# Kernel optimization log

Hardware: AMD Instinct MI355X
Metric: run time of the kernel (lower is better)

Reference implementation:

```python
import jax, jax.numpy as jnp
import numpy as np

N_NODES = 20000
N_EDGES = 640000
NUM_FEATURES = 128
HIDDEN = 256
NUM_CLASSES = 40
EPS = 0.0  # GINConv default eps, not trained


def gin_conv(x, edge_index, W, b):
    # sum-aggregate neighbor features: messages flow src -> dst
    src, dst = edge_index[0], edge_index[1]
    agg = jax.ops.segment_sum(x[src], dst, num_segments=N_NODES)  # [N, d]
    h = (1.0 + EPS) * x + agg
    return h @ W + b


def setup_inputs() -> dict:
    key = jax.random.key(0)
    ks = jax.random.split(key, 10)
    x = jax.random.normal(ks[0], (N_NODES, NUM_FEATURES), dtype=jnp.float32)
    edge_index = jax.random.randint(ks[1], (2, N_EDGES), 0, N_NODES, dtype=jnp.int64)

    def lin(k, fan_in, fan_out):
        kw, kb = jax.random.split(k)
        lim = 1.0 / np.sqrt(fan_in)
        W = jax.random.uniform(kw, (fan_in, fan_out), jnp.float32, -lim, lim)
        b = jax.random.uniform(kb, (fan_out,), jnp.float32, -lim, lim)
        return W, b

    W1, b1 = lin(ks[2], NUM_FEATURES, HIDDEN)
    W2, b2 = lin(ks[3], HIDDEN, HIDDEN)
    W3, b3 = lin(ks[4], HIDDEN, HIDDEN)
    W4, b4 = lin(ks[5], HIDDEN, NUM_CLASSES)
    return {"x": x, "edge_index": edge_index,
            "W1": W1, "b1": b1, "W2": W2, "b2": b2,
            "W3": W3, "b3": b3, "W4": W4, "b4": b4}


def reference(x, edge_index, W1, b1, W2, b2, W3, b3, W4, b4):
    h = jax.nn.relu(gin_conv(x, edge_index, W1, b1))
    h = jax.nn.relu(gin_conv(h, edge_index, W2, b2))
    h = jax.nn.relu(gin_conv(h, edge_index, W3, b3))
    return gin_conv(h, edge_index, W4, b4)
```

## Files before the change

kernel.cpp:

```cpp
#include <hip/hip_runtime.h>

typedef __attribute__((ext_vector_type(8))) short bf16x8;
typedef __attribute__((ext_vector_type(4))) float f32x4;
typedef __attribute__((ext_vector_type(2))) float f32x2;

#define CAP 128

__device__ __forceinline__ ushort f2bf(float f) {
    union { float f; uint u; } c; c.f = f;
    uint u = c.u;
    u += 0x7fffu + ((u >> 16) & 1u);
    return (ushort)(u >> 16);
}
__device__ __forceinline__ f32x2 up2(uint u) {
    union { uint u; float f; } lo, hi;
    lo.u = u << 16; hi.u = u & 0xffff0000u;
    f32x2 r; r.x = lo.f; r.y = hi.f; return r;
}
__device__ __forceinline__ void acc4(f32x2* a, uint4 v) {
    a[0] += up2(v.x); a[1] += up2(v.y); a[2] += up2(v.z); a[3] += up2(v.w);
}

__global__ void zero_kernel(int* __restrict__ p, int n) {
    int i = blockIdx.x * blockDim.x + threadIdx.x;
    if (i < n) p[i] = 0;
}

__global__ void fill_cvt(const int* __restrict__ src, const int* __restrict__ dst,
                         int* __restrict__ cnt, ushort* __restrict__ pcsr, int E,
                         const float* __restrict__ x, ushort* __restrict__ xb, int n4,
                         const float* __restrict__ W1, ushort* __restrict__ W1T,
                         const float* __restrict__ W2, ushort* __restrict__ W2T,
                         const float* __restrict__ W3, ushort* __restrict__ W3T,
                         const float* __restrict__ W4, ushort* __restrict__ W4T) {
    int idx = blockIdx.x * blockDim.x + threadIdx.x;
    if (idx < E) {
        int d = dst[idx];
        int pos = atomicAdd(&cnt[d], 1);
        pcsr[((size_t)d << 7) + pos] = (ushort)src[idx];
        return;
    }
    idx -= E;
    if (idx < n4) {
        float4 v = *(const float4*)&x[(size_t)idx * 4];
        ushort4 o; o.x = f2bf(v.x); o.y = f2bf(v.y); o.z = f2bf(v.z); o.w = f2bf(v.w);
        *(ushort4*)&xb[(size_t)idx * 4] = o;
        return;
    }
    int i = idx - n4;
    if (i < 32768) {
        int n = i & 255, k = i >> 8;
        W1T[n * 128 + k] = f2bf(W1[k * 256 + n]);
    } else if (i < 32768 + 65536) {
        int j = i - 32768; int n = j & 255, k = j >> 8;
        W2T[n * 256 + k] = f2bf(W2[k * 256 + n]);
    } else if (i < 32768 + 131072) {
        int j = i - 98304; int n = j & 255, k = j >> 8;
        W3T[n * 256 + k] = f2bf(W3[k * 256 + n]);
    } else if (i < 32768 + 131072 + 32768) {
        int j = i - 163840; int n = j & 127, k = j >> 7;
        W4T[n * 256 + k] = f2bf(n < 40 ? W4[k * 40 + n] : 0.f);
    }
}

template <int D>
__global__ __launch_bounds__(256) void gather_chunk(
        const ushort* __restrict__ xb, const int* __restrict__ cnt,
        const ushort* __restrict__ pcsr, ushort* __restrict__ h, int N) {
    constexpr int CF = D / 4;
    constexpr int LPN = CF / 8;
    constexpr int NPB = 256 / LPN;
    constexpr int RS = (D == 256) ? 9 : 8;
    int chunk = blockIdx.x & 3;
    int t = threadIdx.x;
    int node = (blockIdx.x >> 2) * NPB + (t / LPN);
    if (node >= N) return;
    int l = t & (LPN - 1);
    uint fo2 = (uint)chunk * (CF * 2) + (uint)l * 16;
    const char* xc = (const char*)xb;
    char* hc = (char*)h;
    int deg = cnt[node];
    const ushort* crow = pcsr + ((size_t)node << 7);
    uint selfoff = ((uint)node << RS) + fo2;

    f32x2 a[4], b[4] = {}, c[4] = {}, d[4] = {};
    {
        uint4 sv = *(const uint4*)(xc + selfoff);
        a[0] = up2(sv.x); a[1] = up2(sv.y); a[2] = up2(sv.z); a[3] = up2(sv.w);
    }
    int e = 0;
    for (; e + 4 <= deg; e += 4) {
        uint s0 = crow[e], s1 = crow[e + 1], s2 = crow[e + 2], s3 = crow[e + 3];
        uint4 v0 = *(const uint4*)(xc + (s0 << RS) + fo2);
        uint4 v1 = *(const uint4*)(xc + (s1 << RS) + fo2);
        uint4 v2 = *(const uint4*)(xc + (s2 << RS) + fo2);
        uint4 v3 = *(const uint4*)(xc + (s3 << RS) + fo2);
        acc4(a, v0); acc4(b, v1); acc4(c, v2); acc4(d, v3);
    }
    for (; e < deg; ++e) {
        uint s = crow[e];
        uint4 v = *(const uint4*)(xc + (s << RS) + fo2);
        acc4(a, v);
    }
    #pragma unroll
    for (int i = 0; i < 4; ++i) a[i] += (b[i] + c[i]) + d[i];
    uint4 o;
    o.x = (uint)f2bf(a[0].x) | ((uint)f2bf(a[0].y) << 16);
    o.y = (uint)f2bf(a[1].x) | ((uint)f2bf(a[1].y) << 16);
    o.z = (uint)f2bf(a[2].x) | ((uint)f2bf(a[2].y) << 16);
    o.w = (uint)f2bf(a[3].x) | ((uint)f2bf(a[3].y) << 16);
    *(uint4*)(hc + selfoff) = o;
}

__global__ __launch_bounds__(256) void gather_out_kernel(
        const ushort* __restrict__ y, const int* __restrict__ cnt,
        const ushort* __restrict__ pcsr, const float* __restrict__ b,
        float* __restrict__ out, int N) {
    int node = blockIdx.x * 32 + (threadIdx.x >> 3);
    if (node >= N) return;
    int l = threadIdx.x & 7;
    uint fo2 = (uint)l * 16;
    const char* yc = (const char*)y;
    int deg = cnt[node];
    const ushort* crow = pcsr + ((size_t)node << 7);

    f32x2 a[4], bb[4] = {}, cc[4] = {}, dd[4] = {};
    {
        uint4 sv = *(const uint4*)(yc + ((uint)node << 7) + fo2);
        a[0] = up2(sv.x); a[1] = up2(sv.y); a[2] = up2(sv.z); a[3] = up2(sv.w);
    }
    int e = 0;
    for (; e + 4 <= deg; e += 4) {
        uint s0 = crow[e], s1 = crow[e + 1], s2 = crow[e + 2], s3 = crow[e + 3];
        uint4 v0 = *(const uint4*)(yc + (s0 << 7) + fo2);
        uint4 v1 = *(const uint4*)(yc + (s1 << 7) + fo2);
        uint4 v2 = *(const uint4*)(yc + (s2 << 7) + fo2);
        uint4 v3 = *(const uint4*)(yc + (s3 << 7) + fo2);
        acc4(a, v0); acc4(bb, v1); acc4(cc, v2); acc4(dd, v3);
    }
    for (; e < deg; ++e) {
        uint s = crow[e];
        uint4 v = *(const uint4*)(yc + (s << 7) + fo2);
        acc4(a, v);
    }
    #pragma unroll
    for (int i = 0; i < 4; ++i) a[i] += (bb[i] + cc[i]) + dd[i];

    if (l < 5) {
        int f = l * 8;
        float4 o0 = make_float4(a[0].x + b[f + 0], a[0].y + b[f + 1],
                                a[1].x + b[f + 2], a[1].y + b[f + 3]);
        float4 o1 = make_float4(a[2].x + b[f + 4], a[2].y + b[f + 5],
                                a[3].x + b[f + 6], a[3].y + b[f + 7]);
        *(float4*)&out[(size_t)node * 40 + f] = o0;
        *(float4*)&out[(size_t)node * 40 + f + 4] = o1;
    }
}

#define GBM 64
#define GBN 128
#define GBK 64
#define LDT 72

template <bool OUTF32, bool RELU>
__global__ __launch_bounds__(256) void mfma_gemm(
        const ushort* __restrict__ A, const ushort* __restrict__ BT,
        const float* __restrict__ bias, void* __restrict__ Cout,
        int M, int Ncols, int K, int Cld) {
    __shared__ __align__(16) ushort As[GBM * LDT];
    __shared__ __align__(16) ushort Bs[GBN * LDT];
    int tid = threadIdx.x;
    int lane = tid & 63;
    int wave = tid >> 6;
    int row0 = blockIdx.x * GBM;
    int col0 = blockIdx.y * GBN;
    int wr = (wave >> 1) * 32;
    int wc = (wave & 1) * 64;
    int sr = tid >> 3;
    int sc = (tid & 7) * 8;
    int rr = lane & 15;
    int kq = (lane >> 4) * 8;
    f32x4 acc[2][4] = {};

    for (int k0 = 0; k0 < K; k0 += GBK) {
        int4 a0 = *(const int4*)&A[(size_t)(row0 + sr) * K + k0 + sc];
        int4 a1 = *(const int4*)&A[(size_t)(row0 + sr + 32) * K + k0 + sc];
        int4 b0 = *(const int4*)&BT[(size_t)(col0 + sr) * K + k0 + sc];
        int4 b1 = *(const int4*)&BT[(size_t)(col0 + sr + 32) * K + k0 + sc];
        int4 b2 = *(const int4*)&BT[(size_t)(col0 + sr + 64) * K + k0 + sc];
        int4 b3 = *(const int4*)&BT[(size_t)(col0 + sr + 96) * K + k0 + sc];
        __syncthreads();
        *(int4*)&As[sr * LDT + sc] = a0;
        *(int4*)&As[(sr + 32) * LDT + sc] = a1;
        *(int4*)&Bs[sr * LDT + sc] = b0;
        *(int4*)&Bs[(sr + 32) * LDT + sc] = b1;
        *(int4*)&Bs[(sr + 64) * LDT + sc] = b2;
        *(int4*)&Bs[(sr + 96) * LDT + sc] = b3;
        __syncthreads();
        #pragma unroll
        for (int kk = 0; kk < 2; ++kk) {
            int kof = kk * 32 + kq;
            bf16x8 af[2], bfr[4];
            #pragma unroll
            for (int i = 0; i < 2; ++i)
                af[i] = *(const bf16x8*)&As[(wr + i * 16 + rr) * LDT + kof];
            #pragma unroll
            for (int j = 0; j < 4; ++j)
                bfr[j] = *(const bf16x8*)&Bs[(wc + j * 16 + rr) * LDT + kof];
            #pragma unroll
            for (int i = 0; i < 2; ++i)
                #pragma unroll
                for (int j = 0; j < 4; ++j)
                    acc[i][j] = __builtin_amdgcn_mfma_f32_16x16x32_bf16(af[i], bfr[j], acc[i][j], 0, 0, 0);
        }
    }

    int rq = (lane >> 4) * 4;
    #pragma unroll
    for (int j = 0; j < 4; ++j) {
        int col = col0 + wc + j * 16 + rr;
        if (col >= Ncols) continue;
        float bv = bias ? bias[col] : 0.f;
        #pragma unroll
        for (int i = 0; i < 2; ++i) {
            #pragma unroll
            for (int r = 0; r < 4; ++r) {
                int row = row0 + wr + i * 16 + rq + r;
                if (row >= M) continue;
                float v = acc[i][j][r] + bv;
                if (RELU) v = fmaxf(v, 0.f);
                if (OUTF32) ((float*)Cout)[(size_t)row * Cld + col] = v;
                else        ((ushort*)Cout)[(size_t)row * Cld + col] = f2bf(v);
            }
        }
    }
}

static inline size_t al256(size_t x) { return (x + 255) & ~(size_t)255; }

extern "C" void kernel_launch(void* const* d_in, const int* in_sizes, int n_in,
                              void* d_out, int out_size, void* d_ws, size_t ws_size,
                              hipStream_t stream) {
    const float* x  = (const float*)d_in[0];
    const int*   ei = (const int*)d_in[1];
    const float* W1 = (const float*)d_in[2];
    const float* b1 = (const float*)d_in[3];
    const float* W2 = (const float*)d_in[4];
    const float* b2 = (const float*)d_in[5];
    const float* W3 = (const float*)d_in[6];
    const float* b3 = (const float*)d_in[7];
    const float* W4 = (const float*)d_in[8];
    const float* b4 = (const float*)d_in[9];
    float* out = (float*)d_out;

    int N = in_sizes[0] / 128;
    int E = in_sizes[1] / 2;
    const int* src = ei;
    const int* dst = ei + E;
    int Mpad = ((N + 127) / 128) * 128;

    char* ws = (char*)d_ws;
    int* cnt       = (int*)ws;
    ushort* pcsr   = (ushort*)(cnt + N);
    size_t off = al256((size_t)N * 4 + (size_t)N * CAP * 2);
    ushort* xb   = (ushort*)(ws + off); off += al256((size_t)N * 128 * 2);
    ushort* bufH = (ushort*)(ws + off); off += al256((size_t)Mpad * 256 * 2);
    ushort* bufA = (ushort*)(ws + off); off += al256((size_t)Mpad * 256 * 2);
    ushort* bufB = (ushort*)(ws + off); off += al256((size_t)Mpad * 256 * 2);
    ushort* bufY = (ushort*)(ws + off); off += al256((size_t)Mpad * 64 * 2);
    ushort* W1T  = (ushort*)(ws + off); off += al256((size_t)256 * 128 * 2);
    ushort* W2T  = (ushort*)(ws + off); off += al256((size_t)256 * 256 * 2);
    ushort* W3T  = (ushort*)(ws + off); off += al256((size_t)256 * 256 * 2);
    ushort* W4T  = (ushort*)(ws + off); off += al256((size_t)128 * 256 * 2);

    zero_kernel<<<(N + 1023) / 1024, 1024, 0, stream>>>(cnt, N);

    int n4 = N * 128 / 4;
    int fcTotal = E + n4 + 196608;
    fill_cvt<<<(fcTotal + 255) / 256, 256, 0, stream>>>(src, dst, cnt, pcsr, E, x, xb, n4,
                                                        W1, W1T, W2, W2T, W3, W3T, W4, W4T);

    int g1Blocks = ((N + 63) / 64) * 4;
    int g2Blocks = ((N + 31) / 32) * 4;
    dim3 gemmGrid(Mpad / GBM, 2);
    dim3 gemmGrid4(Mpad / GBM, 1);

    gather_chunk<128><<<g1Blocks, 256, 0, stream>>>(xb, cnt, pcsr, bufH, N);
    mfma_gemm<false, true><<<gemmGrid, 256, 0, stream>>>(bufH, W1T, b1, bufA, N, 256, 128, 256);
    gather_chunk<256><<<g2Blocks, 256, 0, stream>>>(bufA, cnt, pcsr, bufH, N);
    mfma_gemm<false, true><<<gemmGrid, 256, 0, stream>>>(bufH, W2T, b2, bufB, N, 256, 256, 256);
    gather_chunk<256><<<g2Blocks, 256, 0, stream>>>(bufB, cnt, pcsr, bufH, N);
    mfma_gemm<false, true><<<gemmGrid, 256, 0, stream>>>(bufH, W3T, b3, bufA, N, 256, 256, 256);
    mfma_gemm<false, false><<<gemmGrid4, 256, 0, stream>>>(bufA, W4T, nullptr, bufY, N, 64, 256, 64);
    gather_out_kernel<<<(N + 31) / 32, 256, 0, stream>>>(bufY, cnt, pcsr, b4, out, N);
}
```

Before: 178.4 us.

## Split CSR build atomics into 8 partitioned counters then compact

Edge insertion now spreads atomics over 8 counter partitions chosen by block index, writing into per-partition 32-slot segments. A new compact kernel prefix-sums the partition counts and copies them into the original padded CSR. The aim is to reduce atomic contention on the per-node counters. In exchange it adds a kernel launch, more zeroing and extra memory traffic, and a node can overflow a 32-slot partition segment.

```diff
diff --git a/kernel.cpp b/kernel.cpp
--- a/kernel.cpp
+++ b/kernel.cpp
@@ -5,6 +5,7 @@
 typedef __attribute__((ext_vector_type(2))) float f32x2;
 
 #define CAP 128
+#define SEGC 32
 
 __device__ __forceinline__ ushort f2bf(float f) {
     union { float f; uint u; } c; c.f = f;
@@ -27,7 +28,7 @@
 }
 
 __global__ void fill_cvt(const int* __restrict__ src, const int* __restrict__ dst,
-                         int* __restrict__ cnt, ushort* __restrict__ pcsr, int E,
+                         int* __restrict__ cnt8, ushort* __restrict__ pseg, int E, int N,
                          const float* __restrict__ x, ushort* __restrict__ xb, int n4,
                          const float* __restrict__ W1, ushort* __restrict__ W1T,
                          const float* __restrict__ W2, ushort* __restrict__ W2T,
@@ -35,9 +36,10 @@
                          const float* __restrict__ W4, ushort* __restrict__ W4T) {
     int idx = blockIdx.x * blockDim.x + threadIdx.x;
     if (idx < E) {
+        int p = blockIdx.x & 7;
         int d = dst[idx];
-        int pos = atomicAdd(&cnt[d], 1);
-        pcsr[((size_t)d << 7) + pos] = (ushort)src[idx];
+        int pos = atomicAdd(&cnt8[p * N + d], 1);
+        pseg[((size_t)d << 8) + (p << 5) + pos] = (ushort)src[idx];
         return;
     }
     idx -= E;
@@ -61,6 +63,24 @@
         int j = i - 163840; int n = j & 127, k = j >> 7;
         W4T[n * 256 + k] = f2bf(n < 40 ? W4[k * 40 + n] : 0.f);
     }
+}
+
+__global__ __launch_bounds__(256) void compact_kernel(
+        const int* __restrict__ cnt8, const ushort* __restrict__ pseg,
+        int* __restrict__ cnt, ushort* __restrict__ pcsr, int N) {
+    int node = blockIdx.x * 32 + (threadIdx.x >> 3);
+    if (node >= N) return;
+    int p = threadIdx.x & 7;
+    int c[8];
+    #pragma unroll
+    for (int q = 0; q < 8; ++q) c[q] = cnt8[q * N + node];
+    int pre = 0;
+    #pragma unroll
+    for (int q = 0; q < 8; ++q) if (q < p) pre += c[q];
+    const ushort* srow = pseg + ((size_t)node << 8) + (p << 5);
+    ushort* drow = pcsr + ((size_t)node << 7) + pre;
+    for (int i = 0; i < c[p]; ++i) drow[i] = srow[i];
+    if (p == 7) cnt[node] = pre + c[7];
 }
 
 template <int D>
@@ -260,9 +280,11 @@
     int Mpad = ((N + 127) / 128) * 128;
 
     char* ws = (char*)d_ws;
-    int* cnt       = (int*)ws;
-    ushort* pcsr   = (ushort*)(cnt + N);
-    size_t off = al256((size_t)N * 4 + (size_t)N * CAP * 2);
+    int* cnt8      = (int*)ws;
+    int* cnt       = cnt8 + 8 * N;
+    ushort* pseg   = (ushort*)(cnt + N);
+    ushort* pcsr   = pseg + (size_t)N * 256;
+    size_t off = al256((size_t)(9 * N) * 4 + (size_t)N * 256 * 2 + (size_t)N * CAP * 2);
     ushort* xb   = (ushort*)(ws + off); off += al256((size_t)N * 128 * 2);
     ushort* bufH = (ushort*)(ws + off); off += al256((size_t)Mpad * 256 * 2);
     ushort* bufA = (ushort*)(ws + off); off += al256((size_t)Mpad * 256 * 2);
@@ -273,12 +295,13 @@
     ushort* W3T  = (ushort*)(ws + off); off += al256((size_t)256 * 256 * 2);
     ushort* W4T  = (ushort*)(ws + off); off += al256((size_t)128 * 256 * 2);
 
-    zero_kernel<<<(N + 1023) / 1024, 1024, 0, stream>>>(cnt, N);
+    zero_kernel<<<(8 * N + 1023) / 1024, 1024, 0, stream>>>(cnt8, 8 * N);
 
     int n4 = N * 128 / 4;
     int fcTotal = E + n4 + 196608;
-    fill_cvt<<<(fcTotal + 255) / 256, 256, 0, stream>>>(src, dst, cnt, pcsr, E, x, xb, n4,
+    fill_cvt<<<(fcTotal + 255) / 256, 256, 0, stream>>>(src, dst, cnt8, pseg, E, N, x, xb, n4,
                                                         W1, W1T, W2, W2T, W3, W3T, W4, W4T);
+    compact_kernel<<<(N + 31) / 32, 256, 0, stream>>>(cnt8, pseg, cnt, pcsr, N);
 
     int g1Blocks = ((N + 63) / 64) * 4;
     int g2Blocks = ((N + 31) / 32) * 4;
```

Result: no change. 175.4 us (-1.7%).

## Build padded CSR via two-pass bucketed binning with shared-memory atomics

Applied to the files above, without the earlier changes.

Replaces the zero kernel plus global-atomic CSR fill with a two-pass scheme. First, edge blocks bin edges into 64-node buckets using LDS atomics and write packed (dst,src) pairs to a staging region. Second, one block per bucket scatters them into the padded CSR and writes the counts, so no cnt zeroing is needed. This cuts global atomic contention but adds a staging buffer and an extra launch. It assumes each block-bucket pair holds at most 64 edges and that node ids fit in 16 bits.

```diff
diff --git a/kernel.cpp b/kernel.cpp
--- a/kernel.cpp
+++ b/kernel.cpp
@@ -5,6 +5,9 @@
 typedef __attribute__((ext_vector_type(2))) float f32x2;
 
 #define CAP 128
+#define EB 4096
+#define NBJ 320
+#define BSH 6
 
 __device__ __forceinline__ ushort f2bf(float f) {
     union { float f; uint u; } c; c.f = f;
@@ -21,26 +24,34 @@
     a[0] += up2(v.x); a[1] += up2(v.y); a[2] += up2(v.z); a[3] += up2(v.w);
 }
 
-__global__ void zero_kernel(int* __restrict__ p, int n) {
-    int i = blockIdx.x * blockDim.x + threadIdx.x;
-    if (i < n) p[i] = 0;
-}
-
-__global__ void fill_cvt(const int* __restrict__ src, const int* __restrict__ dst,
-                         int* __restrict__ cnt, ushort* __restrict__ pcsr, int E,
-                         const float* __restrict__ x, ushort* __restrict__ xb, int n4,
-                         const float* __restrict__ W1, ushort* __restrict__ W1T,
-                         const float* __restrict__ W2, ushort* __restrict__ W2T,
-                         const float* __restrict__ W3, ushort* __restrict__ W3T,
-                         const float* __restrict__ W4, ushort* __restrict__ W4T) {
-    int idx = blockIdx.x * blockDim.x + threadIdx.x;
-    if (idx < E) {
-        int d = dst[idx];
-        int pos = atomicAdd(&cnt[d], 1);
-        pcsr[((size_t)d << 7) + pos] = (ushort)src[idx];
+__global__ __launch_bounds__(256) void fill_cvtA(
+        const int* __restrict__ src, const int* __restrict__ dst,
+        uint* __restrict__ region, ushort* __restrict__ cntA, int E, int nAB,
+        const float* __restrict__ x, ushort* __restrict__ xb, int n4,
+        const float* __restrict__ W1, ushort* __restrict__ W1T,
+        const float* __restrict__ W2, ushort* __restrict__ W2T,
+        const float* __restrict__ W3, ushort* __restrict__ W3T,
+        const float* __restrict__ W4, ushort* __restrict__ W4T) {
+    if ((int)blockIdx.x < nAB) {
+        __shared__ uint lcnt[NBJ];
+        int tid = threadIdx.x;
+        for (int i = tid; i < NBJ; i += 256) lcnt[i] = 0;
+        __syncthreads();
+        int b = blockIdx.x;
+        int e0 = b * EB;
+        int eend = e0 + EB < E ? e0 + EB : E;
+        for (int e = e0 + tid; e < eend; e += 256) {
+            uint d = (uint)dst[e];
+            uint s = (uint)src[e];
+            uint j = d >> BSH;
+            uint pos = atomicAdd(&lcnt[j], 1u);
+            region[(((uint)b * NBJ + j) << 6) + pos] = (d << 16) | s;
+        }
+        __syncthreads();
+        for (int i = tid; i < NBJ; i += 256) cntA[(uint)b * NBJ + i] = (ushort)lcnt[i];
         return;
     }
-    idx -= E;
+    int idx = ((int)blockIdx.x - nAB) * 256 + threadIdx.x;
     if (idx < n4) {
         float4 v = *(const float4*)&x[(size_t)idx * 4];
         ushort4 o; o.x = f2bf(v.x); o.y = f2bf(v.y); o.z = f2bf(v.z); o.w = f2bf(v.w);
@@ -61,6 +72,33 @@
         int j = i - 163840; int n = j & 127, k = j >> 7;
         W4T[n * 256 + k] = f2bf(n < 40 ? W4[k * 40 + n] : 0.f);
     }
+}
+
+__global__ __launch_bounds__(256) void buildB(
+        const uint* __restrict__ region, const ushort* __restrict__ cntA,
+        int* __restrict__ cnt, ushort* __restrict__ pcsr, int N, int nAB) {
+    __shared__ uint lcnt[64];
+    __shared__ ushort ca[NBJ];
+    int j = blockIdx.x;
+    int tid = threadIdx.x;
+    if (tid < 64) lcnt[tid] = 0;
+    for (int b = tid; b < nAB; b += 256) ca[b] = cntA[(uint)b * NBJ + j];
+    __syncthreads();
+    int sub = tid >> 6;
+    int i = tid & 63;
+    int nbb = (nAB + 3) >> 2;
+    for (int bb = 0; bb < nbb; ++bb) {
+        int b = bb * 4 + sub;
+        if (b < nAB && i < (int)ca[b]) {
+            uint ev = region[(((uint)b * NBJ + j) << 6) + i];
+            uint d = ev >> 16;
+            uint pos = atomicAdd(&lcnt[d & 63], 1u);
+            pcsr[((size_t)d << 7) + pos] = (ushort)(ev & 0xffffu);
+        }
+    }
+    __syncthreads();
+    int node = (j << BSH) + tid;
+    if (tid < 64 && node < N) cnt[node] = (int)lcnt[tid];
 }
 
 template <int D>
@@ -258,11 +296,16 @@
     const int* src = ei;
     const int* dst = ei + E;
     int Mpad = ((N + 127) / 128) * 128;
+    int nAB = (E + EB - 1) / EB;
+    int NB  = (N + 63) >> BSH;
 
     char* ws = (char*)d_ws;
     int* cnt       = (int*)ws;
     ushort* pcsr   = (ushort*)(cnt + N);
-    size_t off = al256((size_t)N * 4 + (size_t)N * CAP * 2);
+    ushort* cntA   = pcsr + (size_t)N * CAP;
+    uint* region   = (uint*)(cntA + (size_t)nAB * NBJ);
+    size_t off = al256((size_t)N * 4 + (size_t)N * CAP * 2 +
+                       (size_t)nAB * NBJ * 2 + (size_t)nAB * NBJ * 64 * 4);
     ushort* xb   = (ushort*)(ws + off); off += al256((size_t)N * 128 * 2);
     ushort* bufH = (ushort*)(ws + off); off += al256((size_t)Mpad * 256 * 2);
     ushort* bufA = (ushort*)(ws + off); off += al256((size_t)Mpad * 256 * 2);
@@ -273,12 +316,11 @@
     ushort* W3T  = (ushort*)(ws + off); off += al256((size_t)256 * 256 * 2);
     ushort* W4T  = (ushort*)(ws + off); off += al256((size_t)128 * 256 * 2);
 
-    zero_kernel<<<(N + 1023) / 1024, 1024, 0, stream>>>(cnt, N);
-
     int n4 = N * 128 / 4;
-    int fcTotal = E + n4 + 196608;
-    fill_cvt<<<(fcTotal + 255) / 256, 256, 0, stream>>>(src, dst, cnt, pcsr, E, x, xb, n4,
-                                                        W1, W1T, W2, W2T, W3, W3T, W4, W4T);
+    int cvtBlocks = (n4 + 196608 + 255) / 256;
+    fill_cvtA<<<nAB + cvtBlocks, 256, 0, stream>>>(src, dst, region, cntA, E, nAB, x, xb, n4,
+                                                   W1, W1T, W2, W2T, W3, W3T, W4, W4T);
+    buildB<<<NB, 256, 0, stream>>>(region, cntA, cnt, pcsr, N, nAB);
 
     int g1Blocks = ((N + 63) / 64) * 4;
     int g2Blocks = ((N + 31) / 32) * 4;
```

After: 161.9 us. 1.1x faster.
